# Optimization experiments

Measured on AMD Instinct MI355X. Metric: run time of the kernel, lower is better.

## Reference

```python
import jax, jax.numpy as jnp
import numpy as np
from jax import lax

M_POINTS = 512
GRASPNESS_THRESHOLD = 0.1


def setup_inputs() -> dict:
    key = jax.random.key(0)
    k1, k2, k3, k4 = jax.random.split(key, 4)
    B, N, C = 4, 32768, 512
    point_clouds = jax.random.normal(k1, (B, N, 3), dtype=jnp.float32)
    features = jax.random.normal(k2, (B, C, N), dtype=jnp.float32)
    # small scoring heads (GraspableNet 1x1 convs); scale so scores are O(1)
    W_obj = jax.random.normal(k3, (2, C), dtype=jnp.float32) / jnp.sqrt(float(C))
    b_obj = jnp.zeros((2,), dtype=jnp.float32)
    W_grasp = jax.random.normal(k4, (C,), dtype=jnp.float32) / jnp.sqrt(float(C))
    b_grasp = jnp.zeros((1,), dtype=jnp.float32)
    return {"point_clouds": point_clouds, "features": features,
            "W_obj": W_obj, "b_obj": b_obj, "W_grasp": W_grasp, "b_grasp": b_grasp}


def _masked_fps(xyz, mask):
    """Furthest point sampling restricted to masked points.
    xyz: [N,3], mask: [N] bool. Returns [M_POINTS] int32 indices.
    Equivalent to compacting masked points and running standard FPS
    starting from the first valid point (torch FPS starts at index 0).
    """
    neg_inf = jnp.float32(-jnp.inf)
    # invalid points can never be selected
    dist0 = jnp.where(mask, jnp.float32(jnp.inf), neg_inf)  # [N]
    first = jnp.argmax(mask).astype(jnp.int32)  # first valid index

    def step(carry, _):
        dist, last = carry
        d = jnp.sum((xyz - xyz[last]) ** 2, axis=-1)  # [N]
        dist = jnp.minimum(dist, jnp.where(mask, d, neg_inf))
        nxt = jnp.argmax(dist).astype(jnp.int32)
        return (dist, nxt), last

    _, idxs = lax.scan(step, (dist0, first), None, length=M_POINTS)
    return idxs  # [M_POINTS]


def reference(point_clouds, features, W_obj, b_obj, W_grasp, b_grasp):
    # scoring heads (1x1 conv == per-point linear)
    objectness = jnp.einsum('oc,bcn->bon', W_obj, features) + b_obj[None, :, None]  # [B,2,N]
    graspness = jnp.einsum('c,bcn->bn', W_grasp, features) + b_grasp[0]             # [B,N]

    objectness_mask = jnp.argmax(objectness, axis=1) == 1                # [B,N]
    graspness_mask = graspness > GRASPNESS_THRESHOLD                     # [B,N]
    graspable_mask = objectness_mask & graspness_mask                    # [B,N]

    idxs = jax.vmap(_masked_fps)(point_clouds, graspable_mask)           # [B,M] int32

    feat_g = jnp.take_along_axis(features, idxs[:, None, :], axis=2)     # [B,C,M]
    xyz_g = jnp.take_along_axis(point_clouds, idxs[:, :, None], axis=1)  # [B,M,3]
    score_g = jnp.take_along_axis(graspness, idxs, axis=1)               # [B,M]

    # pack all gathered outputs into one tensor: [B, C+3+1, M]
    out = jnp.concatenate([feat_g,
                           jnp.swapaxes(xyz_g, 1, 2),
                           score_g[:, None, :]], axis=1)
    return out
```

## Files before the change

kernel.cpp:

```cpp
#include <hip/hip_runtime.h>
#include <math.h>

#define BB 4
#define NN 32768
#define CC 512
#define MM 512
#define CAP 8192
#define TPB 512
#define KPT (CAP / TPB)
#define NPAIR (KPT / 2)

typedef float f32x2 __attribute__((ext_vector_type(2)));

#define OFF_G      0
#define OFF_MASK   (OFF_G + BB*NN*4)
#define OFF_CNT    (OFF_MASK + BB*NN)
#define OFF_CIDX   (OFF_CNT + 256)
#define OFF_CXYZD  (OFF_CIDX + BB*CAP*4)
#define OFF_IDXSEL (OFF_CXYZD + BB*CAP*16)
#define OFF_DSLOW  (OFF_IDXSEL + BB*MM*4)

__global__ __launch_bounds__(256) void k_score(const float* __restrict__ feat,
                                               const float* __restrict__ Wobj,
                                               const float* __restrict__ bobj,
                                               const float* __restrict__ Wg,
                                               const float* __restrict__ bg,
                                               float* __restrict__ g_out,
                                               unsigned char* __restrict__ mask_out) {
    __shared__ float w0[CC], w1[CC], wg[CC];
    for (int c = threadIdx.x; c < CC; c += 256) {
        w0[c] = Wobj[c];
        w1[c] = Wobj[CC + c];
        wg[c] = Wg[c];
    }
    __syncthreads();
    int b = blockIdx.y;
    int n = blockIdx.x * 256 + threadIdx.x;
    const float* f = feat + (size_t)b * CC * NN + n;
    double a0 = 0.0, a1 = 0.0, ag = 0.0;
#pragma unroll 8
    for (int c = 0; c < CC; c++) {
        double fv = (double)f[(size_t)c * NN];
        a0 += fv * (double)w0[c];
        a1 += fv * (double)w1[c];
        ag += fv * (double)wg[c];
    }
    float o0 = (float)(a0 + (double)bobj[0]);
    float o1 = (float)(a1 + (double)bobj[1]);
    float g  = (float)(ag + (double)bg[0]);
    g_out[b * NN + n] = g;
    mask_out[b * NN + n] = (o1 > o0 && g > 0.1f) ? 1 : 0;
}

__global__ __launch_bounds__(1024) void k_compact(const float* __restrict__ pc,
                                                  const unsigned char* __restrict__ mask,
                                                  int* __restrict__ cnt,
                                                  int* __restrict__ cidx,
                                                  float4* __restrict__ cxyzd) {
    int b = blockIdx.x, tid = threadIdx.x;
    int lane = tid & 63, wv = tid >> 6;
    __shared__ int wcnt[16], woff[16];
    __shared__ int base;
    if (tid == 0) base = 0;
    __syncthreads();
    for (int ch = 0; ch < NN / 1024; ch++) {
        int n = ch * 1024 + tid;
        bool m = mask[(size_t)b * NN + n] != 0;
        unsigned long long bal = __ballot(m);
        int before = __popcll(bal & ((1ull << lane) - 1ull));
        if (lane == 0) wcnt[wv] = __popcll(bal);
        __syncthreads();
        if (tid == 0) {
            int r = base;
            for (int w = 0; w < 16; w++) { woff[w] = r; r += wcnt[w]; }
            base = r;
        }
        __syncthreads();
        if (m) {
            int pos = woff[wv] + before;
            if (pos < CAP) {
                cidx[b * CAP + pos] = n;
                const float* p = pc + ((size_t)b * NN + n) * 3;
                cxyzd[b * CAP + pos] = make_float4(p[0], p[1], p[2], __int_as_float(n));
            }
        }
        __syncthreads();
    }
    if (tid == 0) cnt[b] = base;
}

template<int CTRL, int RMASK>
__device__ __forceinline__ void dpp_key_max(unsigned long long& key) {
    int lo = (int)(unsigned)key;
    int hi = (int)(unsigned)(key >> 32);
    int olo = __builtin_amdgcn_update_dpp(lo, lo, CTRL, RMASK, 0xF, false);
    int ohi = __builtin_amdgcn_update_dpp(hi, hi, CTRL, RMASK, 0xF, false);
    unsigned long long okey = ((unsigned long long)(unsigned)ohi << 32) | (unsigned)olo;
    if (okey > key) key = okey;
}

__global__ __launch_bounds__(TPB, 1) void k_fps(const int* __restrict__ cnt,
                                                const float4* __restrict__ cxyzd_g,
                                                int* __restrict__ idxsel) {
    int b = blockIdx.x, tid = threadIdx.x;
    int nc = cnt[b];
    if (nc == 0) {
        for (int i = tid; i < MM; i += TPB) idxsel[b * MM + i] = 0;
        return;
    }
    if (nc > CAP) return;

    __shared__ float4 xyzc[CAP];
    __shared__ unsigned long long sred[3];

    f32x2 px2[NPAIR], py2[NPAIR], pz2[NPAIR];
    float pd[KPT];
    const float4* src = cxyzd_g + (size_t)b * CAP;
#pragma unroll
    for (int j = 0; j < NPAIR; j++) {
        int p0 = (2 * j) * TPB + tid;
        int p1 = (2 * j + 1) * TPB + tid;
        bool v0 = p0 < nc, v1 = p1 < nc;
        float4 a = v0 ? src[p0] : make_float4(0.f, 0.f, 0.f, 0.f);
        float4 c = v1 ? src[p1] : make_float4(0.f, 0.f, 0.f, 0.f);
        px2[j] = (f32x2){a.x, c.x};
        py2[j] = (f32x2){a.y, c.y};
        pz2[j] = (f32x2){a.z, c.z};
        pd[2 * j]     = v0 ? __builtin_inff() : -__builtin_inff();
        pd[2 * j + 1] = v1 ? __builtin_inff() : -__builtin_inff();
        if (v0) xyzc[p0] = a;
        if (v1) xyzc[p1] = c;
    }
    if (tid == 0) { sred[0] = 0ull; sred[1] = 0ull; sred[2] = 0ull; }
    __syncthreads();

    unsigned ntid = ~(unsigned)tid;
    int last = 0;
    int s = 0;
    for (int it = 0; it < MM; it++) {
        float4 c4 = xyzc[last];
        if (tid == 0) {
            idxsel[b * MM + it] = __float_as_int(c4.w);
            int zs = (s == 2) ? 0 : s + 1;
            sred[zs] = 0ull;
        }
        f32x2 ncx = {-c4.x, -c4.x};
        f32x2 ncy = {-c4.y, -c4.y};
        f32x2 ncz = {-c4.z, -c4.z};

        float bv = -__builtin_inff();
        int bk = 0;
#pragma unroll
        for (int j = 0; j < NPAIR; j++) {
            f32x2 d2, t;
            asm("v_pk_add_f32 %0, %2, %4\n\t"
                "v_pk_add_f32 %1, %3, %5\n\t"
                "v_pk_mul_f32 %0, %0, %0\n\t"
                "v_pk_mul_f32 %1, %1, %1\n\t"
                "v_pk_add_f32 %0, %0, %1\n\t"
                "v_pk_add_f32 %1, %6, %7\n\t"
                "v_pk_mul_f32 %1, %1, %1\n\t"
                "v_pk_add_f32 %0, %0, %1"
                : "=&v"(d2), "=&v"(t)
                : "v"(px2[j]), "v"(py2[j]), "v"(ncx), "v"(ncy), "v"(pz2[j]), "v"(ncz));
            float nd0 = fminf(pd[2 * j], d2.x);
            pd[2 * j] = nd0;
            if (nd0 > bv) { bv = nd0; bk = 2 * j; }
            float nd1 = fminf(pd[2 * j + 1], d2.y);
            pd[2 * j + 1] = nd1;
            if (nd1 > bv) { bv = nd1; bk = 2 * j + 1; }
        }

        unsigned u = (unsigned)__float_as_int(bv);
        unsigned mono = u ^ ((unsigned)(((int)u) >> 31) | 0x80000000u);
        unsigned keylo = ntid - ((unsigned)bk << 9);
        unsigned long long key = ((unsigned long long)mono << 32) | keylo;

        dpp_key_max<0x111, 0xF>(key);
        dpp_key_max<0x112, 0xF>(key);
        dpp_key_max<0x114, 0xF>(key);
        dpp_key_max<0x118, 0xF>(key);
        dpp_key_max<0x142, 0xA>(key);
        dpp_key_max<0x143, 0xC>(key);
        if ((tid & 63) == 63)
            atomicMax(&sred[s], key);
        __syncthreads();

        unsigned long long w = sred[s];
        last = (int)(~(unsigned)w);
        s = (s == 2) ? 0 : s + 1;
    }
}

__global__ __launch_bounds__(1024) void k_fps_slow(const float* __restrict__ pc,
                                                   const unsigned char* __restrict__ mask,
                                                   const int* __restrict__ cnt,
                                                   float* __restrict__ dist,
                                                   int* __restrict__ idxsel) {
    int b = blockIdx.x, tid = threadIdx.x;
    int lane = tid & 63, wv = tid >> 6;
    if (cnt[b] <= CAP) return;
    __shared__ float redv[16];
    __shared__ int   redp[16];
    __shared__ int   bc;
    int firstn = 0x7fffffff;
    for (int n = tid; n < NN; n += 1024) {
        bool m = mask[(size_t)b * NN + n] != 0;
        dist[(size_t)b * NN + n] = m ? __builtin_inff() : -__builtin_inff();
        if (m && firstn == 0x7fffffff) firstn = n;
    }
    for (int off = 32; off >= 1; off >>= 1) {
        int on = __shfl_xor(firstn, off, 64);
        if (on < firstn) firstn = on;
    }
    if (lane == 0) redp[wv] = firstn;
    __syncthreads();
    if (tid < 64) {
        int p2 = (lane < 16) ? redp[lane] : 0x7fffffff;
        for (int off = 8; off >= 1; off >>= 1) {
            int op = __shfl_xor(p2, off, 64);
            if (op < p2) p2 = op;
        }
        if (lane == 0) bc = p2;
    }
    __threadfence_block();
    __syncthreads();
    int last = bc;
    for (int it = 0; it < MM; it++) {
        float cx = pc[((size_t)b * NN + last) * 3 + 0];
        float cy = pc[((size_t)b * NN + last) * 3 + 1];
        float cz = pc[((size_t)b * NN + last) * 3 + 2];
        float bv = -__builtin_inff();
        int bp = 0x7fffffff;
        for (int n = tid; n < NN; n += 1024) {
            float x = pc[((size_t)b * NN + n) * 3 + 0];
            float y = pc[((size_t)b * NN + n) * 3 + 1];
            float z = pc[((size_t)b * NN + n) * 3 + 2];
            float dx = __fsub_rn(x, cx), dy = __fsub_rn(y, cy), dz = __fsub_rn(z, cz);
            float d = __fadd_rn(__fadd_rn(__fmul_rn(dx, dx), __fmul_rn(dy, dy)),
                                __fmul_rn(dz, dz));
            float od = dist[(size_t)b * NN + n];
            float nd = fminf(od, d);
            dist[(size_t)b * NN + n] = nd;
            if (nd > bv) { bv = nd; bp = n; }
        }
        for (int off = 32; off >= 1; off >>= 1) {
            float ov = __shfl_xor(bv, off, 64);
            int   op = __shfl_xor(bp, off, 64);
            if (ov > bv || (ov == bv && op < bp)) { bv = ov; bp = op; }
        }
        if (lane == 0) { redv[wv] = bv; redp[wv] = bp; }
        if (tid == 1023) idxsel[b * MM + it] = last;
        __threadfence_block();
        __syncthreads();
        if (tid < 64) {
            float v2 = (lane < 16) ? redv[lane] : -__builtin_inff();
            int   p2 = (lane < 16) ? redp[lane] : 0x7fffffff;
            for (int off = 8; off >= 1; off >>= 1) {
                float ov = __shfl_xor(v2, off, 64);
                int   op = __shfl_xor(p2, off, 64);
                if (ov > v2 || (ov == v2 && op < p2)) { v2 = ov; p2 = op; }
            }
            if (lane == 0) bc = p2;
        }
        __threadfence_block();
        __syncthreads();
        last = bc;
    }
}

__global__ __launch_bounds__(256) void k_gather(const float* __restrict__ pc,
                                                const float* __restrict__ feat,
                                                const float* __restrict__ g,
                                                const int* __restrict__ idxsel,
                                                float* __restrict__ out) {
    int bc_ = blockIdx.x;
    int b = bc_ / 516;
    int ch = bc_ % 516;
    for (int m = threadIdx.x; m < MM; m += 256) {
        int n = idxsel[b * MM + m];
        float v;
        if (ch < 512) v = feat[((size_t)b * CC + ch) * NN + n];
        else if (ch < 515) v = pc[((size_t)b * NN + n) * 3 + (ch - 512)];
        else v = g[b * NN + n];
        out[((size_t)b * 516 + ch) * MM + m] = v;
    }
}

extern "C" void kernel_launch(void* const* d_in, const int* in_sizes, int n_in,
                              void* d_out, int out_size, void* d_ws, size_t ws_size,
                              hipStream_t stream) {
    const float* pc    = (const float*)d_in[0];
    const float* feat  = (const float*)d_in[1];
    const float* Wobj  = (const float*)d_in[2];
    const float* bobj  = (const float*)d_in[3];
    const float* Wg    = (const float*)d_in[4];
    const float* bg    = (const float*)d_in[5];
    float* out = (float*)d_out;

    char* ws = (char*)d_ws;
    float*         g_buf   = (float*)(ws + OFF_G);
    unsigned char* mask    = (unsigned char*)(ws + OFF_MASK);
    int*           cnt     = (int*)(ws + OFF_CNT);
    int*           cidx    = (int*)(ws + OFF_CIDX);
    float4*        cxyzd   = (float4*)(ws + OFF_CXYZD);
    int*           idxsel  = (int*)(ws + OFF_IDXSEL);
    float*         dslow   = (float*)(ws + OFF_DSLOW);

    k_score<<<dim3(NN / 256, BB), 256, 0, stream>>>(feat, Wobj, bobj, Wg, bg, g_buf, mask);
    k_compact<<<BB, 1024, 0, stream>>>(pc, mask, cnt, cidx, cxyzd);
    k_fps<<<BB, TPB, 0, stream>>>(cnt, cxyzd, idxsel);
    k_fps_slow<<<BB, 1024, 0, stream>>>(pc, mask, cnt, dslow, idxsel);
    k_gather<<<BB * 516, 256, 0, stream>>>(pc, feat, g_buf, idxsel, out);
}
```

Baseline: 637.7 us.

## Vectorize scoring loads and restructure FPS argmax as float-max plus atomicMin broadcast

The scoring kernel now has each thread handle four points, loading float4 and writing four scores and mask bytes, with the grid shrunk by four. The FPS loop drops the 64-bit key DPP reduction and the shared xyz table. It now reduces a plain float max with DPP and max3, then has only the winning threads find their lowest-index point and publish its coordinates and index via 64-bit atomicMin into double-buffered slots. This shortens the per-iteration reduction and removes the dependent LDS lookup of the winner's coordinates, at the cost of a second barrier per iteration and extra registers for the w component.

```diff
diff --git a/kernel.cpp b/kernel.cpp
--- a/kernel.cpp
+++ b/kernel.cpp
@@ -11,6 +11,7 @@
 #define NPAIR (KPT / 2)
 
 typedef float f32x2 __attribute__((ext_vector_type(2)));
+typedef unsigned long long u64;
 
 #define OFF_G      0
 #define OFF_MASK   (OFF_G + BB*NN*4)
@@ -35,21 +36,36 @@
     }
     __syncthreads();
     int b = blockIdx.y;
-    int n = blockIdx.x * 256 + threadIdx.x;
-    const float* f = feat + (size_t)b * CC * NN + n;
-    double a0 = 0.0, a1 = 0.0, ag = 0.0;
+    int n0 = (blockIdx.x * 256 + threadIdx.x) * 4;
+    const float* f = feat + (size_t)b * CC * NN + n0;
+    double a0[4] = {0,0,0,0}, a1[4] = {0,0,0,0}, ag[4] = {0,0,0,0};
 #pragma unroll 8
     for (int c = 0; c < CC; c++) {
-        double fv = (double)f[(size_t)c * NN];
-        a0 += fv * (double)w0[c];
-        a1 += fv * (double)w1[c];
-        ag += fv * (double)wg[c];
-    }
-    float o0 = (float)(a0 + (double)bobj[0]);
-    float o1 = (float)(a1 + (double)bobj[1]);
-    float g  = (float)(ag + (double)bg[0]);
-    g_out[b * NN + n] = g;
-    mask_out[b * NN + n] = (o1 > o0 && g > 0.1f) ? 1 : 0;
+        float4 v = *(const float4*)(f + (size_t)c * NN);
+        double wa = (double)w0[c], wb = (double)w1[c], wc = (double)wg[c];
+        a0[0] += (double)v.x * wa; a0[1] += (double)v.y * wa;
+        a0[2] += (double)v.z * wa; a0[3] += (double)v.w * wa;
+        a1[0] += (double)v.x * wb; a1[1] += (double)v.y * wb;
+        a1[2] += (double)v.z * wb; a1[3] += (double)v.w * wb;
+        ag[0] += (double)v.x * wc; ag[1] += (double)v.y * wc;
+        ag[2] += (double)v.z * wc; ag[3] += (double)v.w * wc;
+    }
+    double db0 = (double)bobj[0], db1 = (double)bobj[1], dbg = (double)bg[0];
+    float4 gv;
+    uchar4 mk;
+    {
+        float o0, o1, g;
+        o0 = (float)(a0[0] + db0); o1 = (float)(a1[0] + db1); g = (float)(ag[0] + dbg);
+        gv.x = g; mk.x = (o1 > o0 && g > 0.1f) ? 1 : 0;
+        o0 = (float)(a0[1] + db0); o1 = (float)(a1[1] + db1); g = (float)(ag[1] + dbg);
+        gv.y = g; mk.y = (o1 > o0 && g > 0.1f) ? 1 : 0;
+        o0 = (float)(a0[2] + db0); o1 = (float)(a1[2] + db1); g = (float)(ag[2] + dbg);
+        gv.z = g; mk.z = (o1 > o0 && g > 0.1f) ? 1 : 0;
+        o0 = (float)(a0[3] + db0); o1 = (float)(a1[3] + db1); g = (float)(ag[3] + dbg);
+        gv.w = g; mk.w = (o1 > o0 && g > 0.1f) ? 1 : 0;
+    }
+    *(float4*)(g_out + b * NN + n0) = gv;
+    *(uchar4*)(mask_out + b * NN + n0) = mk;
 }
 
 __global__ __launch_bounds__(1024) void k_compact(const float* __restrict__ pc,
@@ -90,13 +106,10 @@
 }
 
 template<int CTRL, int RMASK>
-__device__ __forceinline__ void dpp_key_max(unsigned long long& key) {
-    int lo = (int)(unsigned)key;
-    int hi = (int)(unsigned)(key >> 32);
-    int olo = __builtin_amdgcn_update_dpp(lo, lo, CTRL, RMASK, 0xF, false);
-    int ohi = __builtin_amdgcn_update_dpp(hi, hi, CTRL, RMASK, 0xF, false);
-    unsigned long long okey = ((unsigned long long)(unsigned)ohi << 32) | (unsigned)olo;
-    if (okey > key) key = okey;
+__device__ __forceinline__ float dpp_fmax(float v) {
+    int o = __builtin_amdgcn_update_dpp(__float_as_int(v), __float_as_int(v),
+                                        CTRL, RMASK, 0xF, false);
+    return fmaxf(v, __int_as_float(o));
 }
 
 __global__ __launch_bounds__(TPB, 1) void k_fps(const int* __restrict__ cnt,
@@ -110,10 +123,10 @@
     }
     if (nc > CAP) return;
 
-    __shared__ float4 xyzc[CAP];
-    __shared__ unsigned long long sred[3];
-
-    f32x2 px2[NPAIR], py2[NPAIR], pz2[NPAIR];
+    __shared__ float4 redv4[2];
+    __shared__ u64 slots[2][4];
+
+    f32x2 px2[NPAIR], py2[NPAIR], pz2[NPAIR], pw2[NPAIR];
     float pd[KPT];
     const float4* src = cxyzd_g + (size_t)b * CAP;
 #pragma unroll
@@ -126,30 +139,39 @@
         px2[j] = (f32x2){a.x, c.x};
         py2[j] = (f32x2){a.y, c.y};
         pz2[j] = (f32x2){a.z, c.z};
+        pw2[j] = (f32x2){a.w, c.w};
         pd[2 * j]     = v0 ? __builtin_inff() : -__builtin_inff();
         pd[2 * j + 1] = v1 ? __builtin_inff() : -__builtin_inff();
-        if (v0) xyzc[p0] = a;
-        if (v1) xyzc[p1] = c;
-    }
-    if (tid == 0) { sred[0] = 0ull; sred[1] = 0ull; sred[2] = 0ull; }
-    __syncthreads();
-
-    unsigned ntid = ~(unsigned)tid;
-    int last = 0;
-    int s = 0;
+    }
+    if (tid == 0) {
+        slots[0][0] = (u64)(unsigned)__float_as_int(px2[0].x);
+        slots[0][1] = (u64)(unsigned)__float_as_int(py2[0].x);
+        slots[0][2] = (u64)(unsigned)__float_as_int(pz2[0].x);
+        slots[0][3] = (u64)(unsigned)__float_as_int(pw2[0].x);
+    }
+    __syncthreads();
+
+    int cur = 0;
     for (int it = 0; it < MM; it++) {
-        float4 c4 = xyzc[last];
+        u64 q0 = slots[cur][0];
+        u64 q1 = slots[cur][1];
+        u64 q2 = slots[cur][2];
+        u64 q3 = slots[cur][3];
+        float cx = __int_as_float((int)(unsigned)q0);
+        float cy = __int_as_float((int)(unsigned)q1);
+        float cz = __int_as_float((int)(unsigned)q2);
         if (tid == 0) {
-            idxsel[b * MM + it] = __float_as_int(c4.w);
-            int zs = (s == 2) ? 0 : s + 1;
-            sred[zs] = 0ull;
-        }
-        f32x2 ncx = {-c4.x, -c4.x};
-        f32x2 ncy = {-c4.y, -c4.y};
-        f32x2 ncz = {-c4.z, -c4.z};
-
-        float bv = -__builtin_inff();
-        int bk = 0;
+            idxsel[b * MM + it] = (int)(unsigned)q3;
+            slots[cur ^ 1][0] = ~0ull;
+            slots[cur ^ 1][1] = ~0ull;
+            slots[cur ^ 1][2] = ~0ull;
+            slots[cur ^ 1][3] = ~0ull;
+        }
+        f32x2 ncx = {-cx, -cx};
+        f32x2 ncy = {-cy, -cy};
+        f32x2 ncz = {-cz, -cz};
+
+        float bmax = -__builtin_inff();
 #pragma unroll
         for (int j = 0; j < NPAIR; j++) {
             f32x2 d2, t;
@@ -164,31 +186,51 @@
                 : "=&v"(d2), "=&v"(t)
                 : "v"(px2[j]), "v"(py2[j]), "v"(ncx), "v"(ncy), "v"(pz2[j]), "v"(ncz));
             float nd0 = fminf(pd[2 * j], d2.x);
+            float nd1 = fminf(pd[2 * j + 1], d2.y);
             pd[2 * j] = nd0;
-            if (nd0 > bv) { bv = nd0; bk = 2 * j; }
-            float nd1 = fminf(pd[2 * j + 1], d2.y);
             pd[2 * j + 1] = nd1;
-            if (nd1 > bv) { bv = nd1; bk = 2 * j + 1; }
-        }
-
-        unsigned u = (unsigned)__float_as_int(bv);
-        unsigned mono = u ^ ((unsigned)(((int)u) >> 31) | 0x80000000u);
-        unsigned keylo = ntid - ((unsigned)bk << 9);
-        unsigned long long key = ((unsigned long long)mono << 32) | keylo;
-
-        dpp_key_max<0x111, 0xF>(key);
-        dpp_key_max<0x112, 0xF>(key);
-        dpp_key_max<0x114, 0xF>(key);
-        dpp_key_max<0x118, 0xF>(key);
-        dpp_key_max<0x142, 0xA>(key);
-        dpp_key_max<0x143, 0xC>(key);
-        if ((tid & 63) == 63)
-            atomicMax(&sred[s], key);
-        __syncthreads();
-
-        unsigned long long w = sred[s];
-        last = (int)(~(unsigned)w);
-        s = (s == 2) ? 0 : s + 1;
+            asm("v_max3_f32 %0, %1, %2, %3" : "=v"(bmax) : "v"(nd0), "v"(nd1), "v"(bmax));
+        }
+
+        float wmax = bmax;
+        wmax = dpp_fmax<0x111, 0xF>(wmax);
+        wmax = dpp_fmax<0x112, 0xF>(wmax);
+        wmax = dpp_fmax<0x114, 0xF>(wmax);
+        wmax = dpp_fmax<0x118, 0xF>(wmax);
+        wmax = dpp_fmax<0x142, 0xA>(wmax);
+        wmax = dpp_fmax<0x143, 0xC>(wmax);
+        if ((tid & 63) == 63) ((float*)redv4)[tid >> 6] = wmax;
+        __syncthreads();
+
+        float4 ra = redv4[0];
+        float4 rb = redv4[1];
+        float w, m0, m1;
+        asm("v_max3_f32 %0, %1, %2, %3" : "=v"(m0) : "v"(ra.x), "v"(ra.y), "v"(ra.z));
+        asm("v_max3_f32 %0, %1, %2, %3" : "=v"(m1) : "v"(ra.w), "v"(rb.x), "v"(rb.y));
+        asm("v_max3_f32 %0, %1, %2, %3" : "=v"(m0) : "v"(m0), "v"(rb.z), "v"(rb.w));
+        w = fmaxf(m0, m1);
+
+        if (bmax == w) {
+            unsigned p = 0; float sx = 0.f, sy = 0.f, sz = 0.f, sw = 0.f;
+#pragma unroll
+            for (int j = NPAIR - 1; j >= 0; j--) {
+                if (pd[2 * j + 1] == w) {
+                    p = (2 * j + 1) * TPB + tid;
+                    sx = px2[j].y; sy = py2[j].y; sz = pz2[j].y; sw = pw2[j].y;
+                }
+                if (pd[2 * j] == w) {
+                    p = (2 * j) * TPB + tid;
+                    sx = px2[j].x; sy = py2[j].x; sz = pz2[j].x; sw = pw2[j].x;
+                }
+            }
+            u64 hp = (u64)p << 32;
+            atomicMin(&slots[cur ^ 1][0], hp | (unsigned)__float_as_int(sx));
+            atomicMin(&slots[cur ^ 1][1], hp | (unsigned)__float_as_int(sy));
+            atomicMin(&slots[cur ^ 1][2], hp | (unsigned)__float_as_int(sz));
+            atomicMin(&slots[cur ^ 1][3], hp | (unsigned)__float_as_int(sw));
+        }
+        __syncthreads();
+        cur ^= 1;
     }
 }
 
@@ -307,7 +349,7 @@
     int*           idxsel  = (int*)(ws + OFF_IDXSEL);
     float*         dslow   = (float*)(ws + OFF_DSLOW);
 
-    k_score<<<dim3(NN / 256, BB), 256, 0, stream>>>(feat, Wobj, bobj, Wg, bg, g_buf, mask);
+    k_score<<<dim3(NN / 1024, BB), 256, 0, stream>>>(feat, Wobj, bobj, Wg, bg, g_buf, mask);
     k_compact<<<BB, 1024, 0, stream>>>(pc, mask, cnt, cidx, cxyzd);
     k_fps<<<BB, TPB, 0, stream>>>(cnt, cxyzd, idxsel);
     k_fps_slow<<<BB, 1024, 0, stream>>>(pc, mask, cnt, dslow, idxsel);
```

Measured after the change: 757.1 us. 18.7% more time.

## Replace FPS LDS atomicMax reduction with per-wave slots and speculative coordinate fetch

Applied to the files above, without the earlier changes.

In the fast FPS loop, each wave now writes its winning key into a double-buffered per-wave LDS slot instead of doing an atomicMax into a rotating triple buffer. After the barrier every thread reads all eight wave keys. It speculatively loads the coordinates for all eight candidates in parallel with the max reduction, then selects among them, which shortens the serial chain of reduction followed by a dependent LDS load on each iteration. The cost is more LDS reads and VGPRs per iteration and a small tree of compares.

```diff
diff --git a/kernel.cpp b/kernel.cpp
--- a/kernel.cpp
+++ b/kernel.cpp
@@ -11,6 +11,7 @@
 #define NPAIR (KPT / 2)
 
 typedef float f32x2 __attribute__((ext_vector_type(2)));
+typedef unsigned long long u64;
 
 #define OFF_G      0
 #define OFF_MASK   (OFF_G + BB*NN*4)
@@ -90,12 +91,12 @@
 }
 
 template<int CTRL, int RMASK>
-__device__ __forceinline__ void dpp_key_max(unsigned long long& key) {
+__device__ __forceinline__ void dpp_key_max(u64& key) {
     int lo = (int)(unsigned)key;
     int hi = (int)(unsigned)(key >> 32);
     int olo = __builtin_amdgcn_update_dpp(lo, lo, CTRL, RMASK, 0xF, false);
     int ohi = __builtin_amdgcn_update_dpp(hi, hi, CTRL, RMASK, 0xF, false);
-    unsigned long long okey = ((unsigned long long)(unsigned)ohi << 32) | (unsigned)olo;
+    u64 okey = ((u64)(unsigned)ohi << 32) | (unsigned)olo;
     if (okey > key) key = okey;
 }
 
@@ -111,7 +112,7 @@
     if (nc > CAP) return;
 
     __shared__ float4 xyzc[CAP];
-    __shared__ unsigned long long sred[3];
+    __shared__ u64 red[2][8];
 
     f32x2 px2[NPAIR], py2[NPAIR], pz2[NPAIR];
     float pd[KPT];
@@ -131,19 +132,11 @@
         if (v0) xyzc[p0] = a;
         if (v1) xyzc[p1] = c;
     }
-    if (tid == 0) { sred[0] = 0ull; sred[1] = 0ull; sred[2] = 0ull; }
-    __syncthreads();
-
-    unsigned ntid = ~(unsigned)tid;
-    int last = 0;
-    int s = 0;
+    float4 c4 = src[0];
+    __syncthreads();
+
     for (int it = 0; it < MM; it++) {
-        float4 c4 = xyzc[last];
-        if (tid == 0) {
-            idxsel[b * MM + it] = __float_as_int(c4.w);
-            int zs = (s == 2) ? 0 : s + 1;
-            sred[zs] = 0ull;
-        }
+        if (tid == 0) idxsel[b * MM + it] = __float_as_int(c4.w);
         f32x2 ncx = {-c4.x, -c4.x};
         f32x2 ncy = {-c4.y, -c4.y};
         f32x2 ncz = {-c4.z, -c4.z};
@@ -164,17 +157,17 @@
                 : "=&v"(d2), "=&v"(t)
                 : "v"(px2[j]), "v"(py2[j]), "v"(ncx), "v"(ncy), "v"(pz2[j]), "v"(ncz));
             float nd0 = fminf(pd[2 * j], d2.x);
+            float nd1 = fminf(pd[2 * j + 1], d2.y);
             pd[2 * j] = nd0;
+            pd[2 * j + 1] = nd1;
             if (nd0 > bv) { bv = nd0; bk = 2 * j; }
-            float nd1 = fminf(pd[2 * j + 1], d2.y);
-            pd[2 * j + 1] = nd1;
             if (nd1 > bv) { bv = nd1; bk = 2 * j + 1; }
         }
 
         unsigned u = (unsigned)__float_as_int(bv);
         unsigned mono = u ^ ((unsigned)(((int)u) >> 31) | 0x80000000u);
-        unsigned keylo = ntid - ((unsigned)bk << 9);
-        unsigned long long key = ((unsigned long long)mono << 32) | keylo;
+        unsigned keylo = ~((unsigned)(bk * TPB + tid));
+        u64 key = ((u64)mono << 32) | keylo;
 
         dpp_key_max<0x111, 0xF>(key);
         dpp_key_max<0x112, 0xF>(key);
@@ -182,13 +175,34 @@
         dpp_key_max<0x118, 0xF>(key);
         dpp_key_max<0x142, 0xA>(key);
         dpp_key_max<0x143, 0xC>(key);
-        if ((tid & 63) == 63)
-            atomicMax(&sred[s], key);
-        __syncthreads();
-
-        unsigned long long w = sred[s];
-        last = (int)(~(unsigned)w);
-        s = (s == 2) ? 0 : s + 1;
+        if ((tid & 63) == 63) red[it & 1][tid >> 6] = key;
+        __syncthreads();
+
+        const ulonglong2* rp = (const ulonglong2*)red[it & 1];
+        ulonglong2 ra = rp[0], rb = rp[1], rc = rp[2], rd = rp[3];
+        float4 d0 = xyzc[(int)(~(unsigned)ra.x)];
+        float4 d1 = xyzc[(int)(~(unsigned)ra.y)];
+        float4 d2c = xyzc[(int)(~(unsigned)rb.x)];
+        float4 d3 = xyzc[(int)(~(unsigned)rb.y)];
+        float4 d4 = xyzc[(int)(~(unsigned)rc.x)];
+        float4 d5 = xyzc[(int)(~(unsigned)rc.y)];
+        float4 d6 = xyzc[(int)(~(unsigned)rd.x)];
+        float4 d7 = xyzc[(int)(~(unsigned)rd.y)];
+        u64 ka = ra.x; int ia = 0; if (ra.y > ka) { ka = ra.y; ia = 1; }
+        u64 kb = rb.x; int ib = 2; if (rb.y > kb) { kb = rb.y; ib = 3; }
+        u64 kc = rc.x; int ic = 4; if (rc.y > kc) { kc = rc.y; ic = 5; }
+        u64 kd = rd.x; int id = 6; if (rd.y > kd) { kd = rd.y; id = 7; }
+        if (kb > ka) { ka = kb; ia = ib; }
+        if (kd > kc) { kc = kd; ic = id; }
+        if (kc > ka) { ka = kc; ia = ic; }
+        float4 e0, e1, e2, e3, f0, f1;
+        e0 = (ia & 1) ? d1 : d0;
+        e1 = (ia & 1) ? d3 : d2c;
+        e2 = (ia & 1) ? d5 : d4;
+        e3 = (ia & 1) ? d7 : d6;
+        f0 = (ia & 2) ? e1 : e0;
+        f1 = (ia & 2) ? e3 : e2;
+        c4 = (ia & 4) ? f1 : f0;
     }
 }
 
```

New measurement: 690.0 us. +8.2%, slower.
